# Kernel optimization log

Hardware: AMD Instinct MI355X
Metric: run time of the kernel (lower is better)

Reference implementation:

```python
import jax, jax.numpy as jnp
import numpy as np

N = 100000   # nodes
E = 1600000  # edges (avg degree 16)
D = 128      # input feature dim
H = 128      # hidden_channels
O = 64       # out_channels


def _uniform(key, shape, fan_in):
    bound = 1.0 / np.sqrt(fan_in)
    return jax.random.uniform(key, shape, jnp.float32, -bound, bound)


def setup_inputs() -> dict:
    key = jax.random.key(0)
    ks = jax.random.split(key, 9)
    x = jax.random.normal(ks[0], (N, D), jnp.float32)
    edge_index = jax.random.randint(ks[1], (2, E), 0, N, dtype=jnp.int32)
    return {
        "x": x,
        "edge_index": edge_index,
        # layer 1: SAGEConv(D -> H): lin_l (on aggregated neighbors, with bias), lin_r (root)
        "W1l": _uniform(ks[2], (D, H), D),
        "b1": _uniform(ks[3], (H,), D),
        "W1r": _uniform(ks[4], (D, H), D),
        # layer 2: SAGEConv(H -> O)
        "W2l": _uniform(ks[5], (H, O), H),
        "b2": _uniform(ks[6], (O,), H),
        "W2r": _uniform(ks[7], (H, O), H),
    }


def sage_conv(x, edge_index, Wl, b, Wr):
    """PyG SAGEConv with mean aggregation: lin_l(mean_{j in N(i)} x_j) + lin_r(x_i)."""
    src, dst = edge_index[0], edge_index[1]
    n = x.shape[0]
    msg = x[src]                                                 # [E, D] gather
    agg = jax.ops.segment_sum(msg, dst, num_segments=n)         # [N, D] scatter-add
    cnt = jax.ops.segment_sum(jnp.ones((src.shape[0],), x.dtype), dst, num_segments=n)
    agg = agg / jnp.maximum(cnt, 1.0)[:, None]                  # mean; isolated nodes -> 0
    return agg @ Wl + b + x @ Wr


def reference(x, edge_index, W1l, b1, W1r, W2l, b2, W2r):
    h = jax.nn.relu(sage_conv(x, edge_index, W1l, b1, W1r))
    return sage_conv(h, edge_index, W2l, b2, W2r)
```

## Files before the change

### kernel.cpp

```cpp
#include <hip/hip_runtime.h>
#include <stdint.h>

#define NN 100000
#define NE 1600000
#define MAXDEG 64
#define NSLICE 8
#define SLICE_SZ 12500
#define CHUNK 6400

typedef __attribute__((ext_vector_type(8))) short short8;
typedef __attribute__((ext_vector_type(4))) float f32x4;

__device__ __forceinline__ float bflo(unsigned v) { return __uint_as_float(v << 16); }
__device__ __forceinline__ float bfhi(unsigned v) { return __uint_as_float(v & 0xffff0000u); }
__device__ __forceinline__ unsigned short f2bf(float f) {
  unsigned u = __float_as_uint(f);
  u += 0x7fff + ((u >> 16) & 1);
  return (unsigned short)(u >> 16);
}

__global__ __launch_bounds__(256) void build_buckets(const int* __restrict__ src,
                                                     const int* __restrict__ dst,
                                                     int* __restrict__ cnt,
                                                     int* __restrict__ buck) {
  const int slice = blockIdx.x & (NSLICE - 1);
  const int chunk = blockIdx.x >> 3;
  const int c0 = chunk * CHUNK;
  const int lo = slice * SLICE_SZ, hi = lo + SLICE_SZ;
  for (int e = c0 + (int)threadIdx.x * 4; e < c0 + CHUNK; e += 1024) {
    int4 d = *(const int4*)(dst + e);
    int4 s = *(const int4*)(src + e);
    if (d.x >= lo && d.x < hi) { int p = atomicAdd(&cnt[d.x], 1); if (p < MAXDEG) buck[d.x * MAXDEG + p] = s.x; }
    if (d.y >= lo && d.y < hi) { int p = atomicAdd(&cnt[d.y], 1); if (p < MAXDEG) buck[d.y * MAXDEG + p] = s.y; }
    if (d.z >= lo && d.z < hi) { int p = atomicAdd(&cnt[d.z], 1); if (p < MAXDEG) buck[d.z * MAXDEG + p] = s.z; }
    if (d.w >= lo && d.w < hi) { int p = atomicAdd(&cnt[d.w], 1); if (p < MAXDEG) buck[d.w * MAXDEG + p] = s.w; }
  }
}

__global__ __launch_bounds__(256) void to_bf16(const float* __restrict__ x,
                                               unsigned* __restrict__ xb) {
  int i = blockIdx.x * 256 + threadIdx.x;
  if (i >= NN * 32) return;
  float4 v = ((const float4*)x)[i];
  uint2 o;
  o.x = ((unsigned)f2bf(v.y) << 16) | f2bf(v.x);
  o.y = ((unsigned)f2bf(v.w) << 16) | f2bf(v.z);
  ((uint2*)xb)[i] = o;
}

__global__ __launch_bounds__(256) void transpose_w(const float* __restrict__ W1l,
                                                   const float* __restrict__ W1r,
                                                   const float* __restrict__ W2l,
                                                   const float* __restrict__ W2r,
                                                   unsigned short* __restrict__ WT1,
                                                   unsigned short* __restrict__ WT2) {
  int t = blockIdx.x * 256 + threadIdx.x;
  if (t < 128 * 256) {
    int m = t >> 8, k = t & 255;
    float v = (k < 128) ? W1l[k * 128 + m] : W1r[(k - 128) * 128 + m];
    WT1[t] = f2bf(v);
  } else {
    int i = t - 128 * 256;
    if (i < 64 * 256) {
      int m = i >> 8, k = i & 255;
      float v = (k < 128) ? W2l[k * 64 + m] : W2r[(k - 128) * 64 + m];
      WT2[i] = f2bf(v);
    }
  }
}

template <int M, bool RELU, typename OutT>
__global__ __launch_bounds__(256) void sage_fused(const unsigned* __restrict__ xb,
                                                  const int* __restrict__ cnt,
                                                  const int* __restrict__ buck,
                                                  const unsigned short* __restrict__ WT,
                                                  const float* __restrict__ bias,
                                                  OutT* __restrict__ out) {
  __shared__ unsigned short sA[64][136];

  const int t = threadIdx.x;
  const int lane = t & 63;
  const int wv = t >> 6;
  const int node0 = blockIdx.x * 64;
  const int nb = node0 + wv * 16;
  const int g = lane >> 5;
  const int c = lane & 31;

  int slot[16]; int deg[16];
#pragma unroll
  for (int i = 0; i < 16; i++) {
    int node = nb + i;
    if (node < NN) {
      slot[i] = buck[(size_t)node * MAXDEG + lane];
      deg[i]  = cnt[node];
    } else { slot[i] = 0; deg[i] = 0; }
  }

#pragma unroll
  for (int i = 0; i < 16; i++) {
    float a0 = 0.f, a1 = 0.f, a2 = 0.f, a3 = 0.f;
    int d = deg[i] < MAXDEG ? deg[i] : MAXDEG;
    if (d > 0) {
      int last = d - 1;
      for (int p = 0; p < d; p += 16) {
        uint2 v[8];
#pragma unroll
        for (int j = 0; j < 8; j++) {
          int e = p + 2 * j + g;
          int s = __shfl(slot[i], e < last ? e : last, 64);
          v[j] = *(const uint2*)(xb + (size_t)s * 64 + c * 2);
        }
#pragma unroll
        for (int j = 0; j < 8; j++) {
          int e = p + 2 * j + g;
          unsigned w0 = (e <= last) ? v[j].x : 0u;
          unsigned w1 = (e <= last) ? v[j].y : 0u;
          a0 += bflo(w0); a1 += bfhi(w0);
          a2 += bflo(w1); a3 += bfhi(w1);
        }
      }
      a0 += __shfl_xor(a0, 32, 64);
      a1 += __shfl_xor(a1, 32, 64);
      a2 += __shfl_xor(a2, 32, 64);
      a3 += __shfl_xor(a3, 32, 64);
    }
    float inv = 1.f / (float)(deg[i] > 1 ? deg[i] : 1);
    unsigned pk0 = ((unsigned)f2bf(a1 * inv) << 16) | f2bf(a0 * inv);
    unsigned pk1 = ((unsigned)f2bf(a3 * inv) << 16) | f2bf(a2 * inv);
    if (g == 0) {
      uint2 o; o.x = pk0; o.y = pk1;
      *(uint2*)((unsigned*)&sA[wv * 16 + i][0] + 2 * c) = o;
    }
  }

  const int m = lane & 15;
  const int q = lane >> 4;

  f32x4 acc[M / 16];
#pragma unroll
  for (int cc = 0; cc < M / 16; cc++) acc[cc] = {0.f, 0.f, 0.f, 0.f};

  unsigned xr[16];
#pragma unroll
  for (int i = 0; i < 16; i++) {
    int node = nb + i;
    xr[i] = (node < NN) ? xb[(size_t)node * 64 + lane] : 0u;
  }

#pragma unroll
  for (int ks = 0; ks < 4; ks++) {
    short8 a = *(const short8*)&sA[wv * 16 + m][ks * 32 + q * 8];
#pragma unroll
    for (int cc = 0; cc < M / 16; cc++) {
      short8 b = *(const short8*)(WT + (size_t)(cc * 16 + m) * 256 + ks * 32 + q * 8);
      acc[cc] = __builtin_amdgcn_mfma_f32_16x16x32_bf16(a, b, acc[cc], 0, 0, 0);
    }
  }

#pragma unroll
  for (int i = 0; i < 16; i++)
    ((unsigned*)&sA[wv * 16 + i][0])[lane] = xr[i];

#pragma unroll
  for (int ks = 4; ks < 8; ks++) {
    short8 a = *(const short8*)&sA[wv * 16 + m][(ks - 4) * 32 + q * 8];
#pragma unroll
    for (int cc = 0; cc < M / 16; cc++) {
      short8 b = *(const short8*)(WT + (size_t)(cc * 16 + m) * 256 + ks * 32 + q * 8);
      acc[cc] = __builtin_amdgcn_mfma_f32_16x16x32_bf16(a, b, acc[cc], 0, 0, 0);
    }
  }

#pragma unroll
  for (int cc = 0; cc < M / 16; cc++) {
    int col = cc * 16 + m;
    float bc = bias[col];
#pragma unroll
    for (int r = 0; r < 4; r++) {
      int lr = wv * 16 + q * 4 + r;
      float v = acc[cc][r] + bc;
      if (RELU) v = fmaxf(v, 0.f);
      if constexpr (sizeof(OutT) == 2) sA[lr][col] = f2bf(v);
      else ((float*)&sA[lr][0])[col] = v;
    }
  }
#pragma unroll
  for (int it = 0; it < 4; it++) {
    int idx = it * 64 + lane;
    int rr = idx >> 4, ck = idx & 15;
    int node = node0 + wv * 16 + rr;
    if (node < NN) {
      uint4 v = *(const uint4*)((const char*)&sA[wv * 16 + rr][0] + ck * 16);
      *(uint4*)((char*)(out + (size_t)node * M) + ck * 16) = v;
    }
  }
}

extern "C" void kernel_launch(void* const* d_in, const int* in_sizes, int n_in,
                              void* d_out, int out_size, void* d_ws, size_t ws_size,
                              hipStream_t stream) {
  const float* x   = (const float*)d_in[0];
  const int*   ei  = (const int*)d_in[1];
  const float* W1l = (const float*)d_in[2];
  const float* b1  = (const float*)d_in[3];
  const float* W1r = (const float*)d_in[4];
  const float* W2l = (const float*)d_in[5];
  const float* b2  = (const float*)d_in[6];
  const float* W2r = (const float*)d_in[7];
  float* out = (float*)d_out;

  char* ws = (char*)d_ws;
  int* cnt  = (int*)ws;                                   ws += (512 << 10);
  int* buck = (int*)ws;                                   ws += (size_t)NN * MAXDEG * 4;
  unsigned* xbf = (unsigned*)ws;                          ws += (size_t)NN * 64 * 4;
  unsigned* hb = (unsigned*)ws;                           ws += (size_t)NN * 64 * 4;
  unsigned short* WT1 = (unsigned short*)ws;              ws += 128 * 256 * 2;
  unsigned short* WT2 = (unsigned short*)ws;              ws += 64 * 256 * 2;

  const int* src = ei;
  const int* dst = ei + NE;

  hipMemsetAsync(cnt, 0, (size_t)NN * 4, stream);
  build_buckets<<<NSLICE * (NE / CHUNK), 256, 0, stream>>>(src, dst, cnt, buck);
  to_bf16<<<(NN * 32 + 255) / 256, 256, 0, stream>>>(x, xbf);
  transpose_w<<<192, 256, 0, stream>>>(W1l, W1r, W2l, W2r, WT1, WT2);

  sage_fused<128, true, unsigned short><<<(NN + 63) / 64, 256, 0, stream>>>(
      xbf, cnt, buck, WT1, b1, (unsigned short*)hb);

  sage_fused<64, false, float><<<(NN + 63) / 64, 256, 0, stream>>>(
      hb, cnt, buck, WT2, b2, out);
}
```

Baseline: 384.2 us.

## Gather neighbor rows with 16-byte loads and process two nodes per batch

The neighbor aggregation now has 16 lanes cover a 128-wide bf16 row with uint4 loads, so four edges are gathered at once instead of two. Two nodes are processed together, with up to 16 or 32 loads issued before any accumulation, to put more memory requests in flight. This trades more registers (8 accumulators per node, 16 uint4 buffers) and an extra shuffle-reduction stage for higher memory-level parallelism. Occupancy may fall because of the added register pressure.

Measured after the change: 394.9 us. 2.8% more time.

```diff
diff --git a/kernel.cpp b/kernel.cpp
--- a/kernel.cpp
+++ b/kernel.cpp
@@ -83,8 +83,8 @@
   const int wv = t >> 6;
   const int node0 = blockIdx.x * 64;
   const int nb = node0 + wv * 16;
-  const int g = lane >> 5;
-  const int c = lane & 31;
+  const int sub = lane >> 4;
+  const int cl  = lane & 15;
 
   int slot[16]; int deg[16];
 #pragma unroll
@@ -95,43 +95,120 @@
       deg[i]  = cnt[node];
     } else { slot[i] = 0; deg[i] = 0; }
   }
-
-#pragma unroll
-  for (int i = 0; i < 16; i++) {
-    float a0 = 0.f, a1 = 0.f, a2 = 0.f, a3 = 0.f;
-    int d = deg[i] < MAXDEG ? deg[i] : MAXDEG;
-    if (d > 0) {
-      int last = d - 1;
-      for (int p = 0; p < d; p += 16) {
-        uint2 v[8];
-#pragma unroll
-        for (int j = 0; j < 8; j++) {
-          int e = p + 2 * j + g;
-          int s = __shfl(slot[i], e < last ? e : last, 64);
-          v[j] = *(const uint2*)(xb + (size_t)s * 64 + c * 2);
-        }
-#pragma unroll
-        for (int j = 0; j < 8; j++) {
-          int e = p + 2 * j + g;
-          unsigned w0 = (e <= last) ? v[j].x : 0u;
-          unsigned w1 = (e <= last) ? v[j].y : 0u;
-          a0 += bflo(w0); a1 += bfhi(w0);
-          a2 += bflo(w1); a3 += bfhi(w1);
+#pragma unroll
+  for (int i = 0; i < 16; i++)
+    if (deg[i] == 0) slot[i] = 0;
+
+#define ACC8(a, v, q, d)                                                     \
+  {                                                                          \
+    bool ok = (4 * (q) + sub) < (d);                                         \
+    unsigned w0 = ok ? (v).x : 0u, w1 = ok ? (v).y : 0u;                     \
+    unsigned w2 = ok ? (v).z : 0u, w3 = ok ? (v).w : 0u;                     \
+    a[0] += bflo(w0); a[1] += bfhi(w0); a[2] += bflo(w1); a[3] += bfhi(w1);  \
+    a[4] += bflo(w2); a[5] += bfhi(w2); a[6] += bflo(w3); a[7] += bfhi(w3);  \
+  }
+
+#pragma unroll
+  for (int b = 0; b < 8; b++) {
+    const int i0 = 2 * b, i1 = 2 * b + 1;
+    const int dr0 = deg[i0], dr1 = deg[i1];
+    const int d0 = dr0 < MAXDEG ? dr0 : MAXDEG;
+    const int d1 = dr1 < MAXDEG ? dr1 : MAXDEG;
+    const int l0 = d0 > 1 ? d0 - 1 : 0;
+    const int l1 = d1 > 1 ? d1 - 1 : 0;
+
+    uint4 v0[8], v1[8];
+#pragma unroll
+    for (int q = 0; q < 4; q++) {
+      int s = __shfl(slot[i0], min(4 * q + sub, l0), 64);
+      v0[q] = *(const uint4*)(xb + (size_t)s * 64 + cl * 4);
+    }
+#pragma unroll
+    for (int q = 0; q < 4; q++) {
+      int s = __shfl(slot[i1], min(4 * q + sub, l1), 64);
+      v1[q] = *(const uint4*)(xb + (size_t)s * 64 + cl * 4);
+    }
+    const bool big = (d0 > 16) | (d1 > 16);
+    if (big) {
+#pragma unroll
+      for (int q = 4; q < 8; q++) {
+        int s = __shfl(slot[i0], min(4 * q + sub, l0), 64);
+        v0[q] = *(const uint4*)(xb + (size_t)s * 64 + cl * 4);
+      }
+#pragma unroll
+      for (int q = 4; q < 8; q++) {
+        int s = __shfl(slot[i1], min(4 * q + sub, l1), 64);
+        v1[q] = *(const uint4*)(xb + (size_t)s * 64 + cl * 4);
+      }
+    }
+
+    float a0[8] = {0.f, 0.f, 0.f, 0.f, 0.f, 0.f, 0.f, 0.f};
+    float a1[8] = {0.f, 0.f, 0.f, 0.f, 0.f, 0.f, 0.f, 0.f};
+#pragma unroll
+    for (int q = 0; q < 4; q++) ACC8(a0, v0[q], q, d0);
+#pragma unroll
+    for (int q = 0; q < 4; q++) ACC8(a1, v1[q], q, d1);
+    if (big) {
+#pragma unroll
+      for (int q = 4; q < 8; q++) ACC8(a0, v0[q], q, d0);
+#pragma unroll
+      for (int q = 4; q < 8; q++) ACC8(a1, v1[q], q, d1);
+    }
+    if (d0 > 32) {
+      for (int p = 32; p < d0; p += 16) {
+#pragma unroll
+        for (int q = 0; q < 4; q++) {
+          int idx = p + 4 * q + sub;
+          int s = __shfl(slot[i0], idx < l0 ? idx : l0, 64);
+          uint4 v = *(const uint4*)(xb + (size_t)s * 64 + cl * 4);
+          bool ok = idx < d0;
+          unsigned w0 = ok ? v.x : 0u, w1 = ok ? v.y : 0u;
+          unsigned w2 = ok ? v.z : 0u, w3 = ok ? v.w : 0u;
+          a0[0] += bflo(w0); a0[1] += bfhi(w0); a0[2] += bflo(w1); a0[3] += bfhi(w1);
+          a0[4] += bflo(w2); a0[5] += bfhi(w2); a0[6] += bflo(w3); a0[7] += bfhi(w3);
         }
       }
-      a0 += __shfl_xor(a0, 32, 64);
-      a1 += __shfl_xor(a1, 32, 64);
-      a2 += __shfl_xor(a2, 32, 64);
-      a3 += __shfl_xor(a3, 32, 64);
-    }
-    float inv = 1.f / (float)(deg[i] > 1 ? deg[i] : 1);
-    unsigned pk0 = ((unsigned)f2bf(a1 * inv) << 16) | f2bf(a0 * inv);
-    unsigned pk1 = ((unsigned)f2bf(a3 * inv) << 16) | f2bf(a2 * inv);
-    if (g == 0) {
-      uint2 o; o.x = pk0; o.y = pk1;
-      *(uint2*)((unsigned*)&sA[wv * 16 + i][0] + 2 * c) = o;
-    }
-  }
+    }
+    if (d1 > 32) {
+      for (int p = 32; p < d1; p += 16) {
+#pragma unroll
+        for (int q = 0; q < 4; q++) {
+          int idx = p + 4 * q + sub;
+          int s = __shfl(slot[i1], idx < l1 ? idx : l1, 64);
+          uint4 v = *(const uint4*)(xb + (size_t)s * 64 + cl * 4);
+          bool ok = idx < d1;
+          unsigned w0 = ok ? v.x : 0u, w1 = ok ? v.y : 0u;
+          unsigned w2 = ok ? v.z : 0u, w3 = ok ? v.w : 0u;
+          a1[0] += bflo(w0); a1[1] += bfhi(w0); a1[2] += bflo(w1); a1[3] += bfhi(w1);
+          a1[4] += bflo(w2); a1[5] += bfhi(w2); a1[6] += bflo(w3); a1[7] += bfhi(w3);
+        }
+      }
+    }
+
+#pragma unroll
+    for (int k = 0; k < 8; k++) {
+      a0[k] += __shfl_xor(a0[k], 16, 64);
+      a0[k] += __shfl_xor(a0[k], 32, 64);
+      a1[k] += __shfl_xor(a1[k], 16, 64);
+      a1[k] += __shfl_xor(a1[k], 32, 64);
+    }
+    const float inv0 = 1.f / (float)(dr0 > 1 ? dr0 : 1);
+    const float inv1 = 1.f / (float)(dr1 > 1 ? dr1 : 1);
+    if (sub == 0) {
+      uint4 o0, o1;
+      o0.x = ((unsigned)f2bf(a0[1] * inv0) << 16) | f2bf(a0[0] * inv0);
+      o0.y = ((unsigned)f2bf(a0[3] * inv0) << 16) | f2bf(a0[2] * inv0);
+      o0.z = ((unsigned)f2bf(a0[5] * inv0) << 16) | f2bf(a0[4] * inv0);
+      o0.w = ((unsigned)f2bf(a0[7] * inv0) << 16) | f2bf(a0[6] * inv0);
+      *(uint4*)((unsigned short*)&sA[wv * 16 + i0][0] + cl * 8) = o0;
+      o1.x = ((unsigned)f2bf(a1[1] * inv1) << 16) | f2bf(a1[0] * inv1);
+      o1.y = ((unsigned)f2bf(a1[3] * inv1) << 16) | f2bf(a1[2] * inv1);
+      o1.z = ((unsigned)f2bf(a1[5] * inv1) << 16) | f2bf(a1[4] * inv1);
+      o1.w = ((unsigned)f2bf(a1[7] * inv1) << 16) | f2bf(a1[6] * inv1);
+      *(uint4*)((unsigned short*)&sA[wv * 16 + i1][0] + cl * 8) = o1;
+    }
+  }
+#undef ACC8
 
   const int m = lane & 15;
   const int q = lane >> 4;
```
